# Optimization experiments

Measured on AMD Instinct MI355X. Metric: run time of the kernel, lower is better.

The kernel has to match this reference:

```python
import jax, jax.numpy as jnp
import numpy as np

IN_SIZE = 256
HIDDEN = 512
T = 32768


def setup_inputs() -> dict:
    key = jax.random.key(0)
    ks = jax.random.split(key, 6)
    lim_ih = 1.0 / np.sqrt(HIDDEN)
    inp = {
        "input": jax.random.normal(ks[0], (T, IN_SIZE), dtype=jnp.float32),
        "init_hidden": jax.random.normal(ks[1], (HIDDEN,), dtype=jnp.float32),
        # eqx.nn.GRUCell parameters: weight_ih (3H, in), weight_hh (3H, H), bias (3H,), bias_n (H,)
        "weight_ih": jax.random.uniform(ks[2], (3 * HIDDEN, IN_SIZE), minval=-lim_ih, maxval=lim_ih, dtype=jnp.float32),
        "weight_hh": jax.random.uniform(ks[3], (3 * HIDDEN, HIDDEN), minval=-lim_ih, maxval=lim_ih, dtype=jnp.float32),
        "bias": jax.random.uniform(ks[4], (3 * HIDDEN,), minval=-lim_ih, maxval=lim_ih, dtype=jnp.float32),
        "bias_n": jax.random.uniform(ks[5], (HIDDEN,), minval=-lim_ih, maxval=lim_ih, dtype=jnp.float32),
    }
    return inp


def reference(input, init_hidden, weight_ih, weight_hh, bias, bias_n):
    H = init_hidden.shape[0]
    # Precompute all input-side gates in one big GEMM: [T, 3H]
    igates_all = input @ weight_ih.T + bias

    def step(h, ig):
        hg = weight_hh @ h  # [3H]
        ir, iz, inn = ig[:H], ig[H:2 * H], ig[2 * H:]
        hr, hz, hn = hg[:H], hg[H:2 * H], hg[2 * H:]
        reset = jax.nn.sigmoid(ir + hr)
        upd = jax.nn.sigmoid(iz + hz)
        new = jnp.tanh(inn + reset * (hn + bias_n))
        h_new = new + upd * (h - new)
        # rnn_out_o = atleast_2d(h_new) -> (1, H); [..., 0] -> (1,)
        return h_new, h_new[:1]

    _, out = jax.lax.scan(step, init_hidden, igates_all)
    return out  # [T, 1]
```

## Files before the change

kernel.cpp:

```cpp
#include <hip/hip_runtime.h>


#define T_STEPS    32768
#define INSZ       256
#define HSZ        512
#define TPB        1024
#define NWG        32
#define POLL_GUARD 16384

typedef unsigned long long u64;
typedef unsigned int u32;
typedef u32 u32x4 __attribute__((ext_vector_type(4)));
typedef float f32x4 __attribute__((ext_vector_type(4)));
typedef float f32x2 __attribute__((ext_vector_type(2)));

__device__ __forceinline__ float grp_reduce16(float v) {
  v += __shfl_xor(v, 1);
  v += __shfl_xor(v, 2);
  v += __shfl_xor(v, 4);
  v += __shfl_xor(v, 8);
  return v;
}

__device__ __forceinline__ int hpad(int k) { return k + 4 * (k >> 5); }
__device__ __forceinline__ int xpad(int k) { return k + ((k >> 4) << 2); }

__device__ __forceinline__ void st16_sys(u64* p, u32x4 v) {
  asm volatile("global_store_dwordx4 %0, %1, off sc0 sc1" :: "v"(p), "v"(v) : "memory");
}

__global__ void init_comm(u64* __restrict__ comm, const float* __restrict__ h0) {
  int jj = threadIdx.x;
  u32 bits = __float_as_uint(h0[jj]);
  comm[jj]       = (u64)bits;
  comm[HSZ + jj] = 0xFFFFFFFF00000000ull;
}

__launch_bounds__(TPB, 1)
__global__ void gru_persistent(const float* __restrict__ input,
                               const float* __restrict__ init_hidden,
                               const float* __restrict__ w_ih,
                               const float* __restrict__ w_hh,
                               const float* __restrict__ bias,
                               const float* __restrict__ bias_n,
                               u64* __restrict__ comm,
                               float* __restrict__ out)
{
  const int tid = threadIdx.x;
  const int wg  = blockIdx.x;
  const int g   = tid >> 4;
  const int l   = tid & 15;
  const bool mv = (g < 48);
  const int R   = wg * 16 + (g & 15) + 512 * (g >> 4);

  f32x4 whh[8];
  f32x4 wih[4];
  if (mv) {
    const float* rp = w_hh + (size_t)R * HSZ + l * 32;
    #pragma unroll
    for (int c = 0; c < 8; ++c) whh[c] = *(const f32x4*)(rp + c * 4);
    const float* rp2 = w_ih + (size_t)R * INSZ + l * 16;
    #pragma unroll
    for (int c = 0; c < 4; ++c) wih[c] = *(const f32x4*)(rp2 + c * 4);
  }

  float hold = 0.f, b_r = 0.f, b_z = 0.f, b_n = 0.f, bn = 0.f;
  if (tid < 16) {
    const int j = wg * 16 + tid;
    hold = init_hidden[j];
    b_r  = bias[j];
    b_z  = bias[j + 512];
    b_n  = bias[j + 1024];
    bn   = bias_n[j];
  }

  __shared__ float h_lds[2][HSZ + 4 * (HSZ >> 5)];
  __shared__ float gsum[48];
  __shared__ float isum[2][48];
  __shared__ float xstage[INSZ + (INSZ >> 4) * 4];

  if (tid >= 64 && tid < 128) {
    const int s = tid - 64;
    f32x4 v = *(const f32x4*)(input + s * 4);
    *(f32x4*)&xstage[xpad(s * 4)] = v;
  }
  __syncthreads();
  if (mv) {
    float a = 0.f;
    #pragma unroll
    for (int c = 0; c < 4; ++c) {
      f32x4 xv = *(const f32x4*)&xstage[20 * l + 4 * c];
      #pragma unroll
      for (int u = 0; u < 4; ++u) a += wih[c][u] * xv[u];
    }
    a = grp_reduce16(a);
    if (l == 0) isum[0][g] = a;
  }

  const bool poller = (tid >= 768);
  const int  pt     = tid - 768;
  u32x4 pa, pb, pc, pd, win;

#define ISSUE(Rr) \
  asm volatile("global_load_dwordx4 %0, %1, off sc0 sc1" : "=&v"(Rr) : "v"(lp) : "memory")
#define CHECK(Rr) \
  asm volatile("s_waitcnt vmcnt(3)" : "+v"(Rr)); \
  __builtin_amdgcn_sched_barrier(0); \
  if ((Rr[1] == tt && Rr[3] == tt) || --guard == 0) { win = Rr; break; } \
  ISSUE(Rr)

  for (int t = 0; t < T_STEPS; ++t) {
    const int p  = t & 1;
    const u32 tt = (u32)t;

    f32x4 xnew = {0.f, 0.f, 0.f, 0.f};
    if (tid >= 64 && tid < 128) {
      const int tn = (t + 1 < T_STEPS) ? (t + 1) : (T_STEPS - 1);
      xnew = *(const f32x4*)(input + (size_t)tn * INSZ + (tid - 64) * 4);
    }

    if (poller) {
      const u64* lp = comm + (size_t)p * HSZ + 2 * pt;
      ISSUE(pa); ISSUE(pb); ISSUE(pc); ISSUE(pd);
      int guard = POLL_GUARD;
      for (;;) {
        CHECK(pa);
        CHECK(pb);
        CHECK(pc);
        CHECK(pd);
      }
      f32x2 hv;
      hv[0] = __uint_as_float(win[0]);
      hv[1] = __uint_as_float(win[2]);
      *(f32x2*)&h_lds[p][hpad(2 * pt)] = hv;
    }
    __syncthreads();

    if (mv) {
      float a = 0.f;
      const float* hp = &h_lds[p][l * 36];
      #pragma unroll
      for (int c = 0; c < 8; ++c) {
        f32x4 hv4 = *(const f32x4*)(hp + c * 4);
        #pragma unroll
        for (int u = 0; u < 4; ++u) a += whh[c][u] * hv4[u];
      }
      a = grp_reduce16(a);
      if (l == 0) gsum[g] = a;
    }
    if (tid >= 64 && tid < 128) *(f32x4*)&xstage[xpad((tid - 64) * 4)] = xnew;
    __syncthreads();

    if (tid < 16) {
      const int j = tid;
      const float hr = gsum[j], hz = gsum[16 + j], hn = gsum[32 + j];
      const float i_r = isum[p][j], i_z = isum[p][16 + j], i_n = isum[p][32 + j];
      const float reset = __builtin_amdgcn_rcpf(1.0f + __expf(-(i_r + b_r + hr)));
      const float upd   = __builtin_amdgcn_rcpf(1.0f + __expf(-(i_z + b_z + hz)));
      const float e2    = __expf(2.0f * (i_n + b_n + reset * (hn + bn)));
      const float newv  = 1.0f - 2.0f * __builtin_amdgcn_rcpf(1.0f + e2);
      const float hnew  = newv + upd * (hold - newv);
      hold = hnew;
      const float hpair = __shfl(hnew, tid + 1);
      if ((j & 1) == 0) {
        u64* nbuf = comm + (size_t)((t + 1) & 1) * HSZ;
        u32x4 pk;
        pk[0] = __float_as_uint(hnew);  pk[1] = (u32)(t + 1);
        pk[2] = __float_as_uint(hpair); pk[3] = (u32)(t + 1);
        st16_sys(&nbuf[wg * 16 + j], pk);
        if (wg == 0 && j == 0) out[t] = hnew;
      }
    }

    if (mv) {
      float a2 = 0.f;
      #pragma unroll
      for (int c = 0; c < 4; ++c) {
        f32x4 xv = *(const f32x4*)&xstage[20 * l + 4 * c];
        #pragma unroll
        for (int u = 0; u < 4; ++u) a2 += wih[c][u] * xv[u];
      }
      a2 = grp_reduce16(a2);
      if (l == 0) isum[(t + 1) & 1][g] = a2;
    }
  }
#undef ISSUE
#undef CHECK
}

extern "C" void kernel_launch(void* const* d_in, const int* in_sizes, int n_in,
                              void* d_out, int out_size, void* d_ws, size_t ws_size,
                              hipStream_t stream) {
  const float* input  = (const float*)d_in[0];
  const float* h0     = (const float*)d_in[1];
  const float* w_ih   = (const float*)d_in[2];
  const float* w_hh   = (const float*)d_in[3];
  const float* bias   = (const float*)d_in[4];
  const float* bias_n = (const float*)d_in[5];
  float* out = (float*)d_out;
  u64* comm  = (u64*)d_ws;

  hipLaunchKernelGGL(init_comm, dim3(1), dim3(HSZ), 0, stream, comm, h0);
  hipLaunchKernelGGL(gru_persistent, dim3(NWG), dim3(TPB), 0, stream,
                     input, h0, w_ih, w_hh, bias, bias_n, comm, out);
}
```

Before: 51.76 ms.

## Precompute input gates via GEMM and streamline per-step GRU recurrence

Adds a tiled fp32 GEMM that precomputes all input-side gates into workspace, then runs a new persistent recurrence kernel where each wavefront owns one hidden unit and combines its three gate rows via shuffles instead of a shared-memory round trip and extra barrier. Polling loads are issued ahead of the loop, and hidden-state publication uses 8-byte stores. The goal is to shorten the serial per-step latency. It requires a large workspace, falls back to the old kernel otherwise, and adds an upfront GEMM cost plus per-step global loads of the gate values.

After: 94.69 ms. +82.9%, slower.

```diff
diff --git a/kernel.cpp b/kernel.cpp
--- a/kernel.cpp
+++ b/kernel.cpp
@@ -4,13 +4,13 @@
 #define T_STEPS    32768
 #define INSZ       256
 #define HSZ        512
-#define TPB        1024
 #define NWG        32
 #define POLL_GUARD 16384
 
 typedef unsigned long long u64;
 typedef unsigned int u32;
 typedef u32 u32x4 __attribute__((ext_vector_type(4)));
+typedef u32 u32x2 __attribute__((ext_vector_type(2)));
 typedef float f32x4 __attribute__((ext_vector_type(4)));
 typedef float f32x2 __attribute__((ext_vector_type(2)));
 
@@ -23,10 +23,12 @@
 }
 
 __device__ __forceinline__ int hpad(int k) { return k + 4 * (k >> 5); }
-__device__ __forceinline__ int xpad(int k) { return k + ((k >> 4) << 2); }
 
 __device__ __forceinline__ void st16_sys(u64* p, u32x4 v) {
   asm volatile("global_store_dwordx4 %0, %1, off sc0 sc1" :: "v"(p), "v"(v) : "memory");
+}
+__device__ __forceinline__ void st8_sys(u64* p, u32x2 v) {
+  asm volatile("global_store_dwordx2 %0, %1, off sc0 sc1" :: "v"(p), "v"(v) : "memory");
 }
 
 __global__ void init_comm(u64* __restrict__ comm, const float* __restrict__ h0) {
@@ -36,15 +38,168 @@
   comm[HSZ + jj] = 0xFFFFFFFF00000000ull;
 }
 
-__launch_bounds__(TPB, 1)
-__global__ void gru_persistent(const float* __restrict__ input,
-                               const float* __restrict__ init_hidden,
-                               const float* __restrict__ w_ih,
-                               const float* __restrict__ w_hh,
-                               const float* __restrict__ bias,
-                               const float* __restrict__ bias_n,
-                               u64* __restrict__ comm,
-                               float* __restrict__ out)
+__launch_bounds__(256)
+__global__ void igates_gemm(const float* __restrict__ input,
+                            const float* __restrict__ w_ih,
+                            const float* __restrict__ bias,
+                            float* __restrict__ ig)
+{
+  const int t0 = blockIdx.x * 64;
+  const int r0 = blockIdx.y * 64;
+  const int tid = threadIdx.x;
+  const int tx = tid & 15, ty = tid >> 4;
+  __shared__ float As[64][68];
+  __shared__ float Bs[64][68];
+  float acc[4][4] = {};
+  for (int kc = 0; kc < INSZ; kc += 64) {
+    #pragma unroll
+    for (int i = 0; i < 4; ++i) {
+      const int rr = (tid >> 4) + 16 * i;
+      f32x4 av = *(const f32x4*)&input[(size_t)(t0 + rr) * INSZ + kc + tx * 4];
+      *(f32x4*)&As[rr][tx * 4] = av;
+      f32x4 bv = *(const f32x4*)&w_ih[(size_t)(r0 + rr) * INSZ + kc + tx * 4];
+      #pragma unroll
+      for (int ci = 0; ci < 4; ++ci) Bs[tx * 4 + ci][rr] = bv[ci];
+    }
+    __syncthreads();
+    #pragma unroll 16
+    for (int kk = 0; kk < 64; ++kk) {
+      float av[4], bv[4];
+      #pragma unroll
+      for (int a = 0; a < 4; ++a) av[a] = As[ty * 4 + a][kk];
+      #pragma unroll
+      for (int b = 0; b < 4; ++b) bv[b] = Bs[kk][tx * 4 + b];
+      #pragma unroll
+      for (int a = 0; a < 4; ++a)
+        #pragma unroll
+        for (int b = 0; b < 4; ++b) acc[a][b] += av[a] * bv[b];
+    }
+    __syncthreads();
+  }
+  #pragma unroll
+  for (int a = 0; a < 4; ++a) {
+    #pragma unroll
+    for (int b = 0; b < 4; ++b) {
+      const int r = r0 + tx * 4 + b;
+      ig[(size_t)(t0 + ty * 4 + a) * 1536 + r] = acc[a][b] + bias[r];
+    }
+  }
+}
+
+__launch_bounds__(1024, 1)
+__global__ void gru_fast(const float* __restrict__ IG,
+                         const float* __restrict__ init_hidden,
+                         const float* __restrict__ w_hh,
+                         const float* __restrict__ bias_n,
+                         u64* __restrict__ comm,
+                         float* __restrict__ out)
+{
+  const int tid  = threadIdx.x;
+  const int wg   = blockIdx.x;
+  const int w    = tid >> 6;
+  const int lane = tid & 63;
+  const int grp  = lane >> 4;
+  const int l    = lane & 15;
+  const int j    = wg * 16 + w;
+
+  f32x4 whh[8];
+  if (grp < 3) {
+    const float* rp = w_hh + (size_t)(j + 512 * grp) * HSZ + l * 32;
+    #pragma unroll
+    for (int c = 0; c < 8; ++c) whh[c] = *(const f32x4*)(rp + c * 4);
+  }
+  float hold = 0.f, bn_ = 0.f, ig_r = 0.f, ig_z = 0.f, ig_n = 0.f;
+  if (lane == 0) {
+    hold = init_hidden[j];
+    bn_  = bias_n[j];
+    ig_r = IG[j]; ig_z = IG[512 + j]; ig_n = IG[1024 + j];
+  }
+
+  __shared__ float h_lds[2][HSZ + 4 * (HSZ >> 5)];
+
+  u32x4 pa, pb, pc, pd, win;
+  const int pt = w * 16 + l;
+
+#define ISSUE(Rr) \
+  asm volatile("global_load_dwordx4 %0, %1, off sc0 sc1" : "=&v"(Rr) : "v"(lp) : "memory")
+#define CHECK(Rr) \
+  asm volatile("s_waitcnt vmcnt(3)" : "+v"(Rr)); \
+  __builtin_amdgcn_sched_barrier(0); \
+  if ((Rr[1] == tt && Rr[3] == tt) || --guard == 0) { win = Rr; break; } \
+  ISSUE(Rr)
+
+  if (grp == 3) {
+    const u64* lp = comm + 2 * pt;
+    ISSUE(pa); ISSUE(pb); ISSUE(pc); ISSUE(pd);
+  }
+
+  for (int t = 0; t < T_STEPS; ++t) {
+    const int p  = t & 1;
+    const u32 tt = (u32)t;
+
+    if (grp == 3) {
+      const u64* lp = comm + (size_t)p * HSZ + 2 * pt;
+      int guard = POLL_GUARD;
+      win = pa;
+      for (;;) {
+        CHECK(pa);
+        CHECK(pb);
+        CHECK(pc);
+        CHECK(pd);
+      }
+      f32x2 hv;
+      hv[0] = __uint_as_float(win[0]);
+      hv[1] = __uint_as_float(win[2]);
+      *(f32x2*)&h_lds[p][hpad(2 * pt)] = hv;
+    }
+    __syncthreads();
+
+    float a = 0.f;
+    if (grp < 3) {
+      const float* hp = &h_lds[p][l * 36];
+      #pragma unroll
+      for (int c = 0; c < 8; ++c) {
+        f32x4 hv4 = *(const f32x4*)(hp + c * 4);
+        #pragma unroll
+        for (int u = 0; u < 4; ++u) a += whh[c][u] * hv4[u];
+      }
+      a = grp_reduce16(a);
+    }
+    const float hz = __shfl(a, 16);
+    const float hn = __shfl(a, 32);
+
+    if (lane == 0) {
+      const float reset = __builtin_amdgcn_rcpf(1.0f + __expf(-(ig_r + a)));
+      const float upd   = __builtin_amdgcn_rcpf(1.0f + __expf(-(ig_z + hz)));
+      const float e2    = __expf(2.0f * (ig_n + reset * (hn + bn_)));
+      const float newv  = 1.0f - 2.0f * __builtin_amdgcn_rcpf(1.0f + e2);
+      const float hnew  = newv + upd * (hold - newv);
+      hold = hnew;
+      u32x2 pk;
+      pk[0] = __float_as_uint(hnew);
+      pk[1] = (u32)(t + 1);
+      st8_sys(comm + (size_t)((t + 1) & 1) * HSZ + j, pk);
+      if (wg == 0 && w == 0) out[t] = hnew;
+      const size_t base = (size_t)((t + 1 < T_STEPS) ? (t + 1) : t) * 1536;
+      ig_r = IG[base + j]; ig_z = IG[base + 512 + j]; ig_n = IG[base + 1024 + j];
+    }
+  }
+#undef ISSUE
+#undef CHECK
+}
+
+#define TPB_FB 1024
+__device__ __forceinline__ int xpad(int k) { return k + ((k >> 4) << 2); }
+
+__launch_bounds__(TPB_FB, 1)
+__global__ void gru_persistent_fb(const float* __restrict__ input,
+                                  const float* __restrict__ init_hidden,
+                                  const float* __restrict__ w_ih,
+                                  const float* __restrict__ w_hh,
+                                  const float* __restrict__ bias,
+                                  const float* __restrict__ bias_n,
+                                  u64* __restrict__ comm,
+                                  float* __restrict__ out)
 {
   const int tid = threadIdx.x;
   const int wg  = blockIdx.x;
@@ -63,17 +218,13 @@
     #pragma unroll
     for (int c = 0; c < 4; ++c) wih[c] = *(const f32x4*)(rp2 + c * 4);
   }
-
   float hold = 0.f, b_r = 0.f, b_z = 0.f, b_n = 0.f, bn = 0.f;
   if (tid < 16) {
     const int j = wg * 16 + tid;
     hold = init_hidden[j];
-    b_r  = bias[j];
-    b_z  = bias[j + 512];
-    b_n  = bias[j + 1024];
+    b_r  = bias[j]; b_z = bias[j + 512]; b_n = bias[j + 1024];
     bn   = bias_n[j];
   }
-
   __shared__ float h_lds[2][HSZ + 4 * (HSZ >> 5)];
   __shared__ float gsum[48];
   __shared__ float isum[2][48];
@@ -96,7 +247,6 @@
     a = grp_reduce16(a);
     if (l == 0) isum[0][g] = a;
   }
-
   const bool poller = (tid >= 768);
   const int  pt     = tid - 768;
   u32x4 pa, pb, pc, pd, win;
@@ -112,17 +262,16 @@
   for (int t = 0; t < T_STEPS; ++t) {
     const int p  = t & 1;
     const u32 tt = (u32)t;
-
     f32x4 xnew = {0.f, 0.f, 0.f, 0.f};
     if (tid >= 64 && tid < 128) {
       const int tn = (t + 1 < T_STEPS) ? (t + 1) : (T_STEPS - 1);
       xnew = *(const f32x4*)(input + (size_t)tn * INSZ + (tid - 64) * 4);
     }
-
     if (poller) {
       const u64* lp = comm + (size_t)p * HSZ + 2 * pt;
       ISSUE(pa); ISSUE(pb); ISSUE(pc); ISSUE(pd);
       int guard = POLL_GUARD;
+      win = pa;
       for (;;) {
         CHECK(pa);
         CHECK(pb);
@@ -135,7 +284,6 @@
       *(f32x2*)&h_lds[p][hpad(2 * pt)] = hv;
     }
     __syncthreads();
-
     if (mv) {
       float a = 0.f;
       const float* hp = &h_lds[p][l * 36];
@@ -150,7 +298,6 @@
     }
     if (tid >= 64 && tid < 128) *(f32x4*)&xstage[xpad((tid - 64) * 4)] = xnew;
     __syncthreads();
-
     if (tid < 16) {
       const int j = tid;
       const float hr = gsum[j], hz = gsum[16 + j], hn = gsum[32 + j];
@@ -171,7 +318,6 @@
         if (wg == 0 && j == 0) out[t] = hnew;
       }
     }
-
     if (mv) {
       float a2 = 0.f;
       #pragma unroll
@@ -198,9 +344,21 @@
   const float* bias   = (const float*)d_in[4];
   const float* bias_n = (const float*)d_in[5];
   float* out = (float*)d_out;
-  u64* comm  = (u64*)d_ws;
-
-  hipLaunchKernelGGL(init_comm, dim3(1), dim3(HSZ), 0, stream, comm, h0);
-  hipLaunchKernelGGL(gru_persistent, dim3(NWG), dim3(TPB), 0, stream,
-                     input, h0, w_ih, w_hh, bias, bias_n, comm, out);
-}
+
+  const size_t IG_BYTES = (size_t)T_STEPS * 1536 * sizeof(float);
+
+  if (ws_size >= IG_BYTES + 16384) {
+    float* ig  = (float*)d_ws;
+    u64*  comm = (u64*)((char*)d_ws + IG_BYTES);
+    hipLaunchKernelGGL(init_comm, dim3(1), dim3(HSZ), 0, stream, comm, h0);
+    hipLaunchKernelGGL(igates_gemm, dim3(T_STEPS / 64, 1536 / 64), dim3(256),
+                       0, stream, input, w_ih, bias, ig);
+    hipLaunchKernelGGL(gru_fast, dim3(NWG), dim3(1024), 0, stream,
+                       ig, h0, w_hh, bias_n, comm, out);
+  } else {
+    u64* comm = (u64*)d_ws;
+    hipLaunchKernelGGL(init_comm, dim3(1), dim3(HSZ), 0, stream, comm, h0);
+    hipLaunchKernelGGL(gru_persistent_fb, dim3(NWG), dim3(TPB_FB), 0, stream,
+                       input, h0, w_ih, w_hh, bias, bias_n, comm, out);
+  }
+}
```
